# Kernel tuning notes

Hardware: AMD Instinct MI355X
Metric: run time of the kernel (lower is better)

The kernel has to match this reference:

```python
import jax, jax.numpy as jnp
import numpy as np

UNITARY_SIZE = 128  # 2**7, gate acts on 7 qubits
N_QUBITS = 23
GATE_IDCS = [[0,1,2,3,4,5,6],[7,8,9,10,11,12,13],[3,5,7,9,11,13,15],[16,17,18,19,20,21,22]]


def setup_inputs() -> dict:
    key = jax.random.key(0)
    k1, k2 = jax.random.split(key)
    state = jax.random.normal(k1, (2, 2 ** N_QUBITS), dtype=jnp.float32)
    U = jax.random.normal(k2, (len(GATE_IDCS), 2, UNITARY_SIZE, UNITARY_SIZE), dtype=jnp.float32)
    return {"state": state, "U": U}


def _apply_gate(state, Ur, Ui, idcs, n):
    # permutation exactly as in run_circuit: targeted qubits to the front,
    # leading real/imag channel (dim 0) kept in place
    perm = [0] + [q + 1 for q in idcs + [q for q in range(n) if q not in idcs]]
    inv_perm = np.argsort(np.array(perm)).tolist()
    s = state.reshape((2,) + (2,) * n)
    s = jnp.transpose(s, perm)
    s = s.reshape(2, -1, UNITARY_SIZE)  # (channel, M, 128); matmul contracts last dim
    sr, si = s[0], s[1]
    # Karatsuba 3-matmul complex multiply, as in the NKI kernel
    Wr = jnp.einsum('ka,ma->mk', Ur, sr)
    Wi = jnp.einsum('ka,ma->mk', Ui, si)
    SASB = jnp.einsum('ka,ma->mk', Ur + Ui, sr + si)
    real = Wr - Wi
    imag = SASB - Wr - Wi
    # Faithful to the kernel: it stores the imag result into channel 0 and the
    # real result into channel 1 (swapped relative to the input convention).
    s = jnp.stack([imag, real], axis=0)
    s = s.reshape((2,) + (2,) * n)
    s = jnp.transpose(s, inv_perm)
    return s.reshape(2, -1)


def reference(state, U):
    for g, idcs in enumerate(GATE_IDCS):
        state = _apply_gate(state, U[g, 0], U[g, 1], idcs, N_QUBITS)
    return state
```

## Files before the change

kernel.cpp:

```cpp
#include <hip/hip_runtime.h>


typedef __attribute__((ext_vector_type(8))) short bf16x8;
typedef __attribute__((ext_vector_type(4))) short bf16x4;
typedef __attribute__((ext_vector_type(4))) float f32x4;

static constexpr int NSTATE = 1 << 23;

__device__ inline void tsplit(float x, unsigned short& h, unsigned short& l) {
    unsigned int u = __float_as_uint(x);
    h = (unsigned short)(u >> 16);
    float hf = __uint_as_float(u & 0xFFFF0000u);
    l = (unsigned short)(__float_as_uint(x - hf) >> 16);
}

__device__ inline void rsplit(float x, unsigned short& h, unsigned short& l) {
    unsigned int u = __float_as_uint(x);
    unsigned int r = (u + 0x7FFFu + ((u >> 16) & 1u)) >> 16;
    h = (unsigned short)r;
    float hf = __uint_as_float(r << 16);
    unsigned int u2 = __float_as_uint(x - hf);
    l = (unsigned short)((u2 + 0x7FFFu + ((u2 >> 16) & 1u)) >> 16);
}

__device__ inline float wElem(const float* __restrict__ Ug, int kp, int ap) {
    const int co = kp >> 7, ci = ap >> 7;
    const float v = Ug[((co == ci) ? 16384 : 0) + (kp & 127) * 128 + (ap & 127)];
    return (co & ci) ? -v : v;
}

__device__ inline int fragOff(int i, int t) {
    const int frag = (i >> 4) * 8 + (t >> 5);
    const int slot = (i & 15) + 16 * ((t >> 3) & 3);
    return frag * 512 + slot * 8 + (t & 7);
}

__device__ inline int slotSwz(int frag, int slot) {
    return slot ^ ((slot >> 3) & 6) ^ (frag & 7);
}

__global__ __launch_bounds__(256)
void prep_all(const float* __restrict__ U,
              unsigned short* __restrict__ WAh, unsigned short* __restrict__ WAl,
              unsigned short* __restrict__ WBh, unsigned short* __restrict__ WBl) {
    __shared__ float Arow[256];
    const int t = threadIdx.x;
    if (blockIdx.x < 256) {
        const int i = blockIdx.x;
        Arow[t] = wElem(U + 2 * 32768, i, t);
        __syncthreads();
        float r = 0.f;
        #pragma unroll 8
        for (int k = 0; k < 256; ++k)
            r = fmaf(Arow[k], wElem(U + 32768, k, t), r);
        __syncthreads();
        Arow[t] = r;
        __syncthreads();
        float s = 0.f;
        #pragma unroll 8
        for (int k = 0; k < 256; ++k)
            s = fmaf(Arow[k], wElem(U, k, t), s);
        unsigned short h, l;
        rsplit(s, h, l);
        const int off = fragOff(i, t);
        WAh[off] = h; WAl[off] = l;
    } else {
        const int i = blockIdx.x - 256;
        unsigned short h, l;
        rsplit(wElem(U + 3 * 32768, i, t), h, l);
        const int off = fragOff(i, t);
        WBh[off] = h; WBl[off] = l;
    }
}

__global__ __launch_bounds__(512, 4)
void fused7(const float* __restrict__ src, float* __restrict__ dst,
            const unsigned short* __restrict__ WAh, const unsigned short* __restrict__ WAl,
            const unsigned short* __restrict__ WBh, const unsigned short* __restrict__ WBl)
{
    __shared__ unsigned short S[32768];

    const int t    = threadIdx.x;
    const int lane = t & 63;
    const int w    = t >> 6;
    const int col  = lane & 15, quad = lane >> 4;
    const int hidx = blockIdx.x >> 1;
    const int ka0  = (blockIdx.x & 1) * 64;
    const size_t hbase = (size_t)hidx * 16384;

    const int sb = t >> 2;
    const int sa = (t & 3) * 16;

    auto ldChunk = [&](int q, float4* v) {
        const float* p = src + (size_t)(q >> 1) * NSTATE + hbase
                       + (size_t)sb * 128 + (q & 1) * 64 + sa;
        #pragma unroll
        for (int i = 0; i < 4; ++i) v[i] = *(const float4*)(p + i * 4);
    };
    auto stChunk = [&](int q, const float4* v) {
        const int bufH = (q & 1) * 16384;
        #pragma unroll
        for (int g = 0; g < 2; ++g) {
            const int aL = sa + g * 8;
            float f[8];
            *(float4*)&f[0] = v[g * 2];
            *(float4*)&f[4] = v[g * 2 + 1];
            bf16x8 hv, lv;
            #pragma unroll
            for (int i = 0; i < 8; ++i) {
                unsigned short h, l;
                tsplit(f[i], h, l);
                hv[i] = (short)h; lv[i] = (short)l;
            }
            const int frag = (sb >> 4) * 2 + (aL >> 5);
            const int slot = (sb & 15) + 16 * ((aL & 31) >> 3);
            const int off  = bufH + frag * 512 + slotSwz(frag, slot) * 8;
            *(bf16x8*)&S[off] = hv;
            *(bf16x8*)&S[off + 8192] = lv;
        }
    };

    f32x4 acc[8];
    #pragma unroll
    for (int mi = 0; mi < 8; ++mi) acc[mi] = (f32x4)0.f;

    const int kptile = (w >> 2) * 8 + (ka0 >> 4) + (w & 3);

    float4 stA[4], stB[4];
    ldChunk(0, stA);
    stChunk(0, stA);
    ldChunk(1, stB);
    __syncthreads();

    #pragma unroll
    for (int q = 0; q < 4; ++q) {
        const int bufH = (q & 1) * 16384;
        #pragma unroll
        for (int ksc = 0; ksc < 2; ++ksc) {
            const int ks = q * 2 + ksc;
            const int fw = (kptile * 8 + ks) * 512 + lane * 8;
            const bf16x8 bh = *(const bf16x8*)(WAh + fw);
            const bf16x8 bl = *(const bf16x8*)(WAl + fw);
            #pragma unroll
            for (int mi = 0; mi < 8; ++mi) {
                const int frag = mi * 2 + ksc;
                const int fo = bufH + frag * 512 + slotSwz(frag, lane) * 8;
                const bf16x8 ah = *(const bf16x8*)&S[fo];
                const bf16x8 al = *(const bf16x8*)&S[fo + 8192];
                acc[mi] = __builtin_amdgcn_mfma_f32_16x16x32_bf16(ah, bh, acc[mi], 0, 0, 0);
                acc[mi] = __builtin_amdgcn_mfma_f32_16x16x32_bf16(al, bh, acc[mi], 0, 0, 0);
                acc[mi] = __builtin_amdgcn_mfma_f32_16x16x32_bf16(ah, bl, acc[mi], 0, 0, 0);
            }
        }
        if (q == 0) { ldChunk(2, stA); stChunk(1, stB); }
        else if (q == 1) { ldChunk(3, stB); stChunk(2, stA); }
        else if (q == 2) { stChunk(3, stB); }
        __syncthreads();
    }

    #pragma unroll
    for (int mi = 0; mi < 8; ++mi) {
        const int oct   = (mi * 2 + (quad >> 1)) & 3;
        const int frag2 = (w & 3) * 8 + (w >> 2) * 4 + (mi >> 1);
        const int soff  = frag2 * 512 + slotSwz(frag2, col + 16 * oct) * 8 + (quad & 1) * 4;
        unsigned short hh[4], ll[4];
        #pragma unroll
        for (int r = 0; r < 4; ++r) tsplit(acc[mi][r], hh[r], ll[r]);
        bf16x4 hv = { (short)hh[0], (short)hh[1], (short)hh[2], (short)hh[3] };
        bf16x4 lv = { (short)ll[0], (short)ll[1], (short)ll[2], (short)ll[3] };
        *(bf16x4*)&S[soff] = hv;
        *(bf16x4*)&S[16384 + soff] = lv;
    }
    __syncthreads();

    f32x4 acc2[4][2];
    #pragma unroll
    for (int mi = 0; mi < 4; ++mi)
        #pragma unroll
        for (int nj = 0; nj < 2; ++nj) acc2[mi][nj] = (f32x4)0.f;

    #pragma unroll
    for (int ks2 = 0; ks2 < 8; ++ks2) {
        bf16x8 a2h[4], a2l[4];
        #pragma unroll
        for (int mi = 0; mi < 4; ++mi) {
            const int frag = mi * 8 + ks2;
            const int fo = frag * 512 + slotSwz(frag, lane) * 8;
            a2h[mi] = *(const bf16x8*)&S[fo];
            a2l[mi] = *(const bf16x8*)&S[16384 + fo];
        }
        #pragma unroll
        for (int nj = 0; nj < 2; ++nj) {
            const int fo = ((w * 2 + nj) * 8 + ks2) * 512 + lane * 8;
            const bf16x8 bh2 = *(const bf16x8*)(WBh + fo);
            const bf16x8 bl2 = *(const bf16x8*)(WBl + fo);
            #pragma unroll
            for (int mi = 0; mi < 4; ++mi) {
                acc2[mi][nj] = __builtin_amdgcn_mfma_f32_16x16x32_bf16(a2h[mi], bh2, acc2[mi][nj], 0, 0, 0);
                acc2[mi][nj] = __builtin_amdgcn_mfma_f32_16x16x32_bf16(a2l[mi], bh2, acc2[mi][nj], 0, 0, 0);
                acc2[mi][nj] = __builtin_amdgcn_mfma_f32_16x16x32_bf16(a2h[mi], bl2, acc2[mi][nj], 0, 0, 0);
            }
        }
    }

    #pragma unroll
    for (int nj = 0; nj < 2; ++nj) {
        const int nt2  = w * 2 + nj;
        const int chpp = nt2 >> 3, kb = (nt2 & 7) * 16 + col;
        float* o = dst + (size_t)chpp * NSTATE + hbase + (size_t)kb * 128 + ka0;
        #pragma unroll
        for (int mi = 0; mi < 4; ++mi)
            *(float4*)(o + mi * 16 + quad * 4) = *(float4*)&acc2[mi][nj];
    }
}

extern "C" void kernel_launch(void* const* d_in, const int* in_sizes, int n_in,
                              void* d_out, int out_size, void* d_ws, size_t ws_size,
                              hipStream_t stream) {
    const float* state = (const float*)d_in[0];
    const float* U     = (const float*)d_in[1];
    float* out = (float*)d_out;

    unsigned short* WAh = (unsigned short*)d_ws;
    unsigned short* WAl = WAh + 65536;
    unsigned short* WBh = WAh + 2 * 65536;
    unsigned short* WBl = WAh + 3 * 65536;

    prep_all<<<512, 256, 0, stream>>>(U, WAh, WAl, WBh, WBl);
    fused7 <<<1024, 512, 0, stream>>>(state, out, WAh, WAl, WBh, WBl);
}
```

Before: 166.8 us.

## Double-buffer weight fragment loads and remap block ids across XCDs

Weight fragments for both MFMA stages are now held in double-buffered registers, so the loads for step k+2 are issued while step k computes instead of sitting on the critical path. The A-operand LDS reads are split into halves of four, and the second chunk's global load is issued before the first chunk is converted and stored. Block ids are remapped so consecutive logical blocks land on different XCDs. The cost is higher register pressure under the 512x4 launch bound, which could cause spills or lower occupancy.

```diff
diff --git a/kernel.cpp b/kernel.cpp
--- a/kernel.cpp
+++ b/kernel.cpp
@@ -74,7 +74,7 @@
 }
 
 __global__ __launch_bounds__(512, 4)
-void fused7(const float* __restrict__ src, float* __restrict__ dst,
+void fused8(const float* __restrict__ src, float* __restrict__ dst,
             const unsigned short* __restrict__ WAh, const unsigned short* __restrict__ WAl,
             const unsigned short* __restrict__ WBh, const unsigned short* __restrict__ WBl)
 {
@@ -84,8 +84,10 @@
     const int lane = t & 63;
     const int w    = t >> 6;
     const int col  = lane & 15, quad = lane >> 4;
-    const int hidx = blockIdx.x >> 1;
-    const int ka0  = (blockIdx.x & 1) * 64;
+
+    const int sbid = (blockIdx.x & 7) * 128 + (blockIdx.x >> 3);
+    const int hidx = sbid >> 1;
+    const int ka0  = (sbid & 1) * 64;
     const size_t hbase = (size_t)hidx * 16384;
 
     const int sb = t >> 2;
@@ -120,16 +122,24 @@
         }
     };
 
+    const int kptile = (w >> 2) * 8 + (ka0 >> 4) + (w & 3);
+
     f32x4 acc[8];
     #pragma unroll
     for (int mi = 0; mi < 8; ++mi) acc[mi] = (f32x4)0.f;
-
-    const int kptile = (w >> 2) * 8 + (ka0 >> 4) + (w & 3);
 
     float4 stA[4], stB[4];
     ldChunk(0, stA);
+    ldChunk(1, stB);
+
+    bf16x8 wh[2], wl[2];
+    #pragma unroll
+    for (int i = 0; i < 2; ++i) {
+        const int fw = (kptile * 8 + i) * 512 + lane * 8;
+        wh[i] = *(const bf16x8*)(WAh + fw);
+        wl[i] = *(const bf16x8*)(WAl + fw);
+    }
     stChunk(0, stA);
-    ldChunk(1, stB);
     __syncthreads();
 
     #pragma unroll
@@ -137,19 +147,30 @@
         const int bufH = (q & 1) * 16384;
         #pragma unroll
         for (int ksc = 0; ksc < 2; ++ksc) {
-            const int ks = q * 2 + ksc;
-            const int fw = (kptile * 8 + ks) * 512 + lane * 8;
-            const bf16x8 bh = *(const bf16x8*)(WAh + fw);
-            const bf16x8 bl = *(const bf16x8*)(WAl + fw);
-            #pragma unroll
-            for (int mi = 0; mi < 8; ++mi) {
-                const int frag = mi * 2 + ksc;
-                const int fo = bufH + frag * 512 + slotSwz(frag, lane) * 8;
-                const bf16x8 ah = *(const bf16x8*)&S[fo];
-                const bf16x8 al = *(const bf16x8*)&S[fo + 8192];
-                acc[mi] = __builtin_amdgcn_mfma_f32_16x16x32_bf16(ah, bh, acc[mi], 0, 0, 0);
-                acc[mi] = __builtin_amdgcn_mfma_f32_16x16x32_bf16(al, bh, acc[mi], 0, 0, 0);
-                acc[mi] = __builtin_amdgcn_mfma_f32_16x16x32_bf16(ah, bl, acc[mi], 0, 0, 0);
+            const int ks  = q * 2 + ksc;
+            const int cur = ks & 1;
+            bf16x8 ah[4], al[4];
+            #pragma unroll
+            for (int half = 0; half < 2; ++half) {
+                #pragma unroll
+                for (int mi = 0; mi < 4; ++mi) {
+                    const int frag = (half * 4 + mi) * 2 + ksc;
+                    const int fo = bufH + frag * 512 + slotSwz(frag, lane) * 8;
+                    ah[mi] = *(const bf16x8*)&S[fo];
+                    al[mi] = *(const bf16x8*)&S[fo + 8192];
+                }
+                #pragma unroll
+                for (int mi = 0; mi < 4; ++mi) {
+                    f32x4& a = acc[half * 4 + mi];
+                    a = __builtin_amdgcn_mfma_f32_16x16x32_bf16(ah[mi], wh[cur], a, 0, 0, 0);
+                    a = __builtin_amdgcn_mfma_f32_16x16x32_bf16(al[mi], wh[cur], a, 0, 0, 0);
+                    a = __builtin_amdgcn_mfma_f32_16x16x32_bf16(ah[mi], wl[cur], a, 0, 0, 0);
+                }
+            }
+            if (ks < 6) {
+                const int fw = (kptile * 8 + ks + 2) * 512 + lane * 8;
+                wh[cur] = *(const bf16x8*)(WAh + fw);
+                wl[cur] = *(const bf16x8*)(WAl + fw);
             }
         }
         if (q == 0) { ldChunk(2, stA); stChunk(1, stB); }
@@ -157,6 +178,16 @@
         else if (q == 2) { stChunk(3, stB); }
         __syncthreads();
     }
+
+    bf16x8 wbh[2][2], wbl[2][2];
+    #pragma unroll
+    for (int i = 0; i < 2; ++i)
+        #pragma unroll
+        for (int nj = 0; nj < 2; ++nj) {
+            const int fo = ((w * 2 + nj) * 8 + i) * 512 + lane * 8;
+            wbh[i][nj] = *(const bf16x8*)(WBh + fo);
+            wbl[i][nj] = *(const bf16x8*)(WBl + fo);
+        }
 
     #pragma unroll
     for (int mi = 0; mi < 8; ++mi) {
@@ -181,6 +212,7 @@
 
     #pragma unroll
     for (int ks2 = 0; ks2 < 8; ++ks2) {
+        const int cur = ks2 & 1;
         bf16x8 a2h[4], a2l[4];
         #pragma unroll
         for (int mi = 0; mi < 4; ++mi) {
@@ -190,15 +222,20 @@
             a2l[mi] = *(const bf16x8*)&S[16384 + fo];
         }
         #pragma unroll
-        for (int nj = 0; nj < 2; ++nj) {
-            const int fo = ((w * 2 + nj) * 8 + ks2) * 512 + lane * 8;
-            const bf16x8 bh2 = *(const bf16x8*)(WBh + fo);
-            const bf16x8 bl2 = *(const bf16x8*)(WBl + fo);
+        for (int nj = 0; nj < 2; ++nj)
             #pragma unroll
             for (int mi = 0; mi < 4; ++mi) {
-                acc2[mi][nj] = __builtin_amdgcn_mfma_f32_16x16x32_bf16(a2h[mi], bh2, acc2[mi][nj], 0, 0, 0);
-                acc2[mi][nj] = __builtin_amdgcn_mfma_f32_16x16x32_bf16(a2l[mi], bh2, acc2[mi][nj], 0, 0, 0);
-                acc2[mi][nj] = __builtin_amdgcn_mfma_f32_16x16x32_bf16(a2h[mi], bl2, acc2[mi][nj], 0, 0, 0);
+                f32x4& a = acc2[mi][nj];
+                a = __builtin_amdgcn_mfma_f32_16x16x32_bf16(a2h[mi], wbh[cur][nj], a, 0, 0, 0);
+                a = __builtin_amdgcn_mfma_f32_16x16x32_bf16(a2l[mi], wbh[cur][nj], a, 0, 0, 0);
+                a = __builtin_amdgcn_mfma_f32_16x16x32_bf16(a2h[mi], wbl[cur][nj], a, 0, 0, 0);
+            }
+        if (ks2 < 6) {
+            #pragma unroll
+            for (int nj = 0; nj < 2; ++nj) {
+                const int fo = ((w * 2 + nj) * 8 + ks2 + 2) * 512 + lane * 8;
+                wbh[cur][nj] = *(const bf16x8*)(WBh + fo);
+                wbl[cur][nj] = *(const bf16x8*)(WBl + fo);
             }
         }
     }
@@ -227,5 +264,5 @@
     unsigned short* WBl = WAh + 3 * 65536;
 
     prep_all<<<512, 256, 0, stream>>>(U, WAh, WAl, WBh, WBl);
-    fused7 <<<1024, 512, 0, stream>>>(state, out, WAh, WAl, WBh, WBl);
-}
+    fused8 <<<1024, 512, 0, stream>>>(state, out, WAh, WAl, WBh, WBl);
+}
```

Result: faster. 159.5 us (-4.4%).
